# Performance work log

Hardware: AMD Instinct MI355X
Metric: run time of the kernel (lower is better)

The kernel has to match this reference:

```python
import jax, jax.numpy as jnp
import numpy as np

NUM_QUBITS = 13
NUM_LAYERS = 2


def setup_inputs() -> dict:
    key = jax.random.key(0)
    k1, k2 = jax.random.split(key)
    x = jax.random.normal(k1, (512, 2 ** NUM_QUBITS), dtype=jnp.float32)
    weights = jax.random.normal(k2, (NUM_LAYERS, NUM_QUBITS, 3), dtype=jnp.float32)
    return {"x": x, "weights": weights}


def _rot_matrix(phi, theta, omega):
    # qml.Rot(phi, theta, omega) = RZ(omega) @ RY(theta) @ RZ(phi)
    c = jnp.cos(theta * 0.5).astype(jnp.complex64)
    s = jnp.sin(theta * 0.5).astype(jnp.complex64)
    e_m = jnp.exp((-0.5j) * (phi + omega).astype(jnp.complex64))
    e_p = jnp.exp((0.5j) * (phi + omega).astype(jnp.complex64))
    e_d = jnp.exp((0.5j) * (phi - omega).astype(jnp.complex64))
    e_dc = jnp.exp((-0.5j) * (phi - omega).astype(jnp.complex64))
    row0 = jnp.stack([e_m * c, -e_d * s])
    row1 = jnp.stack([e_dc * s, e_p * c])
    return jnp.stack([row0, row1])  # (2, 2) complex64


def _apply_1q(psi, U, q):
    # psi: (B, 2, 2, ..., 2); contract qubit axis q with 2x2 gate U
    ax = 1 + q
    psi = jnp.moveaxis(psi, ax, -1)
    psi = psi @ U.T
    return jnp.moveaxis(psi, -1, ax)


def _apply_cnot(psi, c, t):
    # X on target where control bit == 1
    s0 = jax.lax.index_in_dim(psi, 0, axis=1 + c, keepdims=True)
    s1 = jax.lax.index_in_dim(psi, 1, axis=1 + c, keepdims=True)
    s1 = jnp.flip(s1, axis=1 + t)
    return jnp.concatenate([s0, s1], axis=1 + c)


def reference(x, weights):
    n = NUM_QUBITS
    B = x.shape[0]
    # AmplitudeEmbedding with normalize=True
    norm = jnp.sqrt(jnp.sum(x * x, axis=1, keepdims=True))
    psi = (x / norm).astype(jnp.complex64).reshape((B,) + (2,) * n)
    # StronglyEntanglingLayers (default ranges r_l = (l % (n-1)) + 1, CNOT imprimitive)
    for l in range(NUM_LAYERS):
        r = (l % (n - 1)) + 1
        for q in range(n):
            U = _rot_matrix(weights[l, q, 0], weights[l, q, 1], weights[l, q, 2])
            psi = _apply_1q(psi, U, q)
        for q in range(n):
            psi = _apply_cnot(psi, q, (q + r) % n)
    # expval(PauliZ(n // 2)) = p(bit=0) - p(bit=1)
    m = n // 2
    probs = jnp.real(psi) ** 2 + jnp.imag(psi) ** 2
    axes = tuple(i for i in range(1, n + 1) if i != 1 + m)
    p = probs.sum(axis=axes)  # (B, 2)
    return p[:, 0] - p[:, 1]
```

## Files before the change

kernel.cpp:

```cpp
#include <hip/hip_runtime.h>
#include <math.h>

#define NQ    13
#define DIM   8192
#define BLOCK 256
#define NGATE 26

#define SW_PAD(i) ((i) + (((i) >> 5) << 2))
#define LDS_N (DIM + 4 * (DIM / 32))

struct PCols { int c[NQ]; };
constexpr PCols make_cols(int r) {
    PCols P{};
    for (int b = 0; b < NQ; ++b) {
        int cc = 1 << b;
        for (int cq = 0; cq < NQ; ++cq) {
            const int cb = 12 - cq;
            const int tb = 12 - ((cq + r) % NQ);
            cc ^= ((cc >> cb) & 1) << tb;
        }
        P.c[b] = cc;
    }
    return P;
}
constexpr PCols C1 = make_cols(1);
constexpr PCols C2 = make_cols(2);
constexpr int make_rm6() {
    int m = 0;
    for (int b = 0; b < NQ; ++b) m |= ((make_cols(2).c[b] >> 6) & 1) << b;
    return m;
}
constexpr int RM6 = make_rm6();

template<int P>
__device__ __forceinline__ void rot32(float* vr, float* vi, const float* __restrict__ g) {
    const float u00r = g[0], u00i = g[1], u01r = g[2], u01i = g[3];
    const float u10r = g[4], u10i = g[5], u11r = g[6], u11i = g[7];
    #pragma unroll
    for (int m = 0; m < 16; ++m) {
        const int j0 = ((m >> P) << (P + 1)) | (m & ((1 << P) - 1));
        const int j1 = j0 | (1 << P);
        const float a0r = vr[j0], a0i = vi[j0];
        const float a1r = vr[j1], a1i = vi[j1];
        vr[j0] = u00r * a0r - u00i * a0i + u01r * a1r - u01i * a1i;
        vi[j0] = u00r * a0i + u00i * a0r + u01r * a1i + u01i * a1r;
        vr[j1] = u10r * a0r - u10i * a0i + u11r * a1r - u11i * a1i;
        vi[j1] = u10r * a0i + u10i * a0r + u11r * a1i + u11i * a1r;
    }
}

__device__ __forceinline__ void lds_load8x4(const float* arr, int base, int step, float* v) {
    #pragma unroll
    for (int g = 0; g < 8; ++g) {
        const float4 t = *(const float4*)&arr[base + step * g];
        v[4*g+0] = t.x; v[4*g+1] = t.y; v[4*g+2] = t.z; v[4*g+3] = t.w;
    }
}
__device__ __forceinline__ void lds_store8x4(float* arr, int base, int step, const float* v) {
    #pragma unroll
    for (int g = 0; g < 8; ++g) {
        float4 t;
        t.x = v[4*g+0]; t.y = v[4*g+1]; t.z = v[4*g+2]; t.w = v[4*g+3];
        *(float4*)&arr[base + step * g] = t;
    }
}

__global__ __launch_bounds__(BLOCK, 1) void qsim_kernel(
    const float* __restrict__ x,
    const float* __restrict__ w,
    float* __restrict__ out)
{
    __shared__ float re[LDS_N];
    __shared__ float im[LDS_N];
    __shared__ float gm[NGATE * 8];
    __shared__ float red[BLOCK / 64];

    const int b   = blockIdx.x;
    const int tid = threadIdx.x;

    if (tid < NGATE) {
        const float phi   = w[tid * 3 + 0];
        const float theta = w[tid * 3 + 1];
        const float omega = w[tid * 3 + 2];
        float c, s;  sincosf(0.5f * theta, &s, &c);
        float sps, cps, sds, cds;
        sincosf(0.5f * (phi + omega), &sps, &cps);
        sincosf(0.5f * (phi - omega), &sds, &cds);
        float* g = &gm[tid * 8];
        g[0] =  cps * c;  g[1] = -sps * c;
        g[2] = -cds * s;  g[3] = -sds * s;
        g[4] =  cds * s;  g[5] = -sds * s;
        g[6] =  cps * c;  g[7] =  sps * c;
    }

    const float4* x4 = (const float4*)(x + (size_t)b * DIM);
    float ss = 0.f;
    #pragma unroll
    for (int k = 0; k < 8; ++k) {
        const int m = tid + BLOCK * k;
        const int a = SW_PAD(m * 4);
        const float4 v = x4[m];
        *(float4*)&re[a] = v;
        *(float4*)&im[a] = make_float4(0.f, 0.f, 0.f, 0.f);
        ss += v.x * v.x + v.y * v.y + v.z * v.z + v.w * v.w;
    }
    #pragma unroll
    for (int off = 32; off > 0; off >>= 1) ss += __shfl_down(ss, off, 64);
    if ((tid & 63) == 0) red[tid >> 6] = ss;
    __syncthreads();
    const float total = red[0] + red[1] + red[2] + red[3];

    float vr[32], vi[32];
    const int baseA = 36 * tid;
    const int baseB = (tid >> 5) * 1152 + (tid & 31);
    const int baseC = 4 * tid + 4 * (tid >> 3);

    lds_load8x4(re, baseA, 4, vr);  lds_load8x4(im, baseA, 4, vi);
    rot32<0>(vr, vi, &gm[(0*13+12)*8]);
    rot32<1>(vr, vi, &gm[(0*13+11)*8]);
    rot32<2>(vr, vi, &gm[(0*13+10)*8]);
    rot32<3>(vr, vi, &gm[(0*13+ 9)*8]);
    rot32<4>(vr, vi, &gm[(0*13+ 8)*8]);
    lds_store8x4(re, baseA, 4, vr); lds_store8x4(im, baseA, 4, vi);
    __syncthreads();

    #pragma unroll
    for (int j = 0; j < 32; ++j) { vr[j] = re[baseB + 36*j]; vi[j] = im[baseB + 36*j]; }
    rot32<0>(vr, vi, &gm[(0*13+7)*8]);
    rot32<1>(vr, vi, &gm[(0*13+6)*8]);
    rot32<2>(vr, vi, &gm[(0*13+5)*8]);
    rot32<3>(vr, vi, &gm[(0*13+4)*8]);
    rot32<4>(vr, vi, &gm[(0*13+3)*8]);
    #pragma unroll
    for (int j = 0; j < 32; ++j) { re[baseB + 36*j] = vr[j]; im[baseB + 36*j] = vi[j]; }
    __syncthreads();

    lds_load8x4(re, baseC, 1152, vr);  lds_load8x4(im, baseC, 1152, vi);
    rot32<2>(vr, vi, &gm[(0*13+2)*8]);
    rot32<3>(vr, vi, &gm[(0*13+1)*8]);
    rot32<4>(vr, vi, &gm[(0*13+0)*8]);
    __syncthreads();
    {
        int tbase = 0;
        #pragma unroll
        for (int bb = 2; bb < 10; ++bb) if ((tid >> (bb - 2)) & 1) tbase ^= C1.c[bb];
        #pragma unroll
        for (int j = 0; j < 32; ++j) {
            int dest = tbase;
            if (j & 1)  dest ^= C1.c[0];
            if (j & 2)  dest ^= C1.c[1];
            if (j & 4)  dest ^= C1.c[10];
            if (j & 8)  dest ^= C1.c[11];
            if (j & 16) dest ^= C1.c[12];
            const int a = SW_PAD(dest);
            re[a] = vr[j]; im[a] = vi[j];
        }
    }
    __syncthreads();

    lds_load8x4(re, baseA, 4, vr);  lds_load8x4(im, baseA, 4, vi);
    rot32<0>(vr, vi, &gm[(1*13+12)*8]);
    rot32<1>(vr, vi, &gm[(1*13+11)*8]);
    rot32<2>(vr, vi, &gm[(1*13+10)*8]);
    rot32<3>(vr, vi, &gm[(1*13+ 9)*8]);
    rot32<4>(vr, vi, &gm[(1*13+ 8)*8]);
    lds_store8x4(re, baseA, 4, vr); lds_store8x4(im, baseA, 4, vi);
    __syncthreads();

    #pragma unroll
    for (int j = 0; j < 32; ++j) { vr[j] = re[baseB + 36*j]; vi[j] = im[baseB + 36*j]; }
    rot32<0>(vr, vi, &gm[(1*13+7)*8]);
    rot32<1>(vr, vi, &gm[(1*13+6)*8]);
    rot32<2>(vr, vi, &gm[(1*13+5)*8]);
    rot32<3>(vr, vi, &gm[(1*13+4)*8]);
    rot32<4>(vr, vi, &gm[(1*13+3)*8]);
    #pragma unroll
    for (int j = 0; j < 32; ++j) { re[baseB + 36*j] = vr[j]; im[baseB + 36*j] = vi[j]; }
    __syncthreads();

    lds_load8x4(re, baseC, 1152, vr);  lds_load8x4(im, baseC, 1152, vi);
    rot32<2>(vr, vi, &gm[(1*13+2)*8]);
    rot32<3>(vr, vi, &gm[(1*13+1)*8]);
    rot32<4>(vr, vi, &gm[(1*13+0)*8]);

    float acc = 0.f;
    #pragma unroll
    for (int jh = 0; jh < 8; ++jh) {
        #pragma unroll
        for (int jl = 0; jl < 4; ++jl) {
            const int j = jh * 4 + jl;
            const int i = (jh << 10) | (tid << 2) | jl;
            const float pr = vr[j] * vr[j] + vi[j] * vi[j];
            acc += (__popc(i & RM6) & 1) ? -pr : pr;
        }
    }
    #pragma unroll
    for (int off = 32; off > 0; off >>= 1) acc += __shfl_down(acc, off, 64);
    __syncthreads();
    if ((tid & 63) == 0) red[tid >> 6] = acc;
    __syncthreads();
    if (tid == 0) out[b] = (red[0] + red[1] + red[2] + red[3]) / total;
}

extern "C" void kernel_launch(void* const* d_in, const int* in_sizes, int n_in,
                              void* d_out, int out_size, void* d_ws, size_t ws_size,
                              hipStream_t stream) {
    const float* x = (const float*)d_in[0];
    const float* w = (const float*)d_in[1];
    float* out = (float*)d_out;
    const int B = in_sizes[0] / DIM;
    qsim_kernel<<<B, BLOCK, 0, stream>>>(x, w, out);
}
```

Baseline: 88.97 us.

## Rewrite statevector kernel with 512 threads, XOR swizzle, DPP lane gates, separate gate prep

Doubles the block to 512 threads with 16 amplitudes per thread and applies two qubits per pass through DPP lane exchanges instead of holding them in registers. The padded LDS layout becomes an XOR swizzle, and the pass structure is redone to fit the new mapping. Gate matrices are now built in a separate prep kernel into workspace and read from global memory, with launch bounds allowing 4 blocks per CU. This targets register pressure and occupancy at the cost of a second launch and more cross-lane shuffles.

```diff
diff --git a/kernel.cpp b/kernel.cpp
--- a/kernel.cpp
+++ b/kernel.cpp
@@ -3,11 +3,13 @@
 
 #define NQ    13
 #define DIM   8192
-#define BLOCK 256
+#define BLOCK 512
 #define NGATE 26
 
-#define SW_PAD(i) ((i) + (((i) >> 5) << 2))
-#define LDS_N (DIM + 4 * (DIM / 32))
+__device__ __forceinline__ int SWZ(int i) {
+    return i ^ (((((i >> 4) ^ (i >> 6)) & 3)) << 2)
+             ^ ((((i >> 10) ^ (i >> 11)) & 1) << 4);
+}
 
 struct PCols { int c[NQ]; };
 constexpr PCols make_cols(int r) {
@@ -24,7 +26,6 @@
     return P;
 }
 constexpr PCols C1 = make_cols(1);
-constexpr PCols C2 = make_cols(2);
 constexpr int make_rm6() {
     int m = 0;
     for (int b = 0; b < NQ; ++b) m |= ((make_cols(2).c[b] >> 6) & 1) << b;
@@ -32,73 +33,147 @@
 }
 constexpr int RM6 = make_rm6();
 
+struct Combos { int k[16]; };
+constexpr Combos make_combos() {
+    Combos K{};
+    for (int j = 0; j < 16; ++j)
+        K.k[j] = ((j & 1) ? C1.c[0] : 0) ^ ((j & 2) ? C1.c[1] : 0)
+               ^ ((j & 4) ? C1.c[2] : 0) ^ ((j & 8) ? C1.c[12] : 0);
+    return K;
+}
+constexpr Combos KC = make_combos();
+
+struct G8 { float4 a, b; };
+
 template<int P>
-__device__ __forceinline__ void rot32(float* vr, float* vi, const float* __restrict__ g) {
-    const float u00r = g[0], u00i = g[1], u01r = g[2], u01i = g[3];
-    const float u10r = g[4], u10i = g[5], u11r = g[6], u11i = g[7];
-    #pragma unroll
-    for (int m = 0; m < 16; ++m) {
+__device__ __forceinline__ void rot16(float* vr, float* vi, const G8 g) {
+    #pragma unroll
+    for (int m = 0; m < 8; ++m) {
         const int j0 = ((m >> P) << (P + 1)) | (m & ((1 << P) - 1));
         const int j1 = j0 | (1 << P);
         const float a0r = vr[j0], a0i = vi[j0];
         const float a1r = vr[j1], a1i = vi[j1];
-        vr[j0] = u00r * a0r - u00i * a0i + u01r * a1r - u01i * a1i;
-        vi[j0] = u00r * a0i + u00i * a0r + u01r * a1i + u01i * a1r;
-        vr[j1] = u10r * a0r - u10i * a0i + u11r * a1r - u11i * a1i;
-        vi[j1] = u10r * a0i + u10i * a0r + u11r * a1i + u11i * a1r;
-    }
-}
-
-__device__ __forceinline__ void lds_load8x4(const float* arr, int base, int step, float* v) {
-    #pragma unroll
-    for (int g = 0; g < 8; ++g) {
-        const float4 t = *(const float4*)&arr[base + step * g];
-        v[4*g+0] = t.x; v[4*g+1] = t.y; v[4*g+2] = t.z; v[4*g+3] = t.w;
-    }
-}
-__device__ __forceinline__ void lds_store8x4(float* arr, int base, int step, const float* v) {
-    #pragma unroll
-    for (int g = 0; g < 8; ++g) {
-        float4 t;
-        t.x = v[4*g+0]; t.y = v[4*g+1]; t.z = v[4*g+2]; t.w = v[4*g+3];
-        *(float4*)&arr[base + step * g] = t;
-    }
-}
-
-__global__ __launch_bounds__(BLOCK, 1) void qsim_kernel(
-    const float* __restrict__ x,
-    const float* __restrict__ w,
-    float* __restrict__ out)
-{
-    __shared__ float re[LDS_N];
-    __shared__ float im[LDS_N];
-    __shared__ float gm[NGATE * 8];
-    __shared__ float red[BLOCK / 64];
-
-    const int b   = blockIdx.x;
-    const int tid = threadIdx.x;
-
-    if (tid < NGATE) {
-        const float phi   = w[tid * 3 + 0];
-        const float theta = w[tid * 3 + 1];
-        const float omega = w[tid * 3 + 2];
+        vr[j0] = g.a.x * a0r - g.a.y * a0i + g.a.z * a1r - g.a.w * a1i;
+        vi[j0] = g.a.x * a0i + g.a.y * a0r + g.a.z * a1i + g.a.w * a1r;
+        vr[j1] = g.b.x * a0r - g.b.y * a0i + g.b.z * a1r - g.b.w * a1i;
+        vi[j1] = g.b.x * a0i + g.b.y * a0r + g.b.z * a1i + g.b.w * a1r;
+    }
+}
+
+template<int CTRL>
+__device__ __forceinline__ float dppx(float v) {
+    return __int_as_float(
+        __builtin_amdgcn_update_dpp(0, __float_as_int(v), CTRL, 0xf, 0xf, true));
+}
+
+template<int CTRL>
+__device__ __forceinline__ void rotlane16(float* vr, float* vi, const G8 g, const bool hi) {
+    const float Ar = hi ? g.b.z : g.a.x;
+    const float Ai = hi ? g.b.w : g.a.y;
+    const float Br = hi ? g.b.x : g.a.z;
+    const float Bi = hi ? g.b.y : g.a.w;
+    #pragma unroll
+    for (int j = 0; j < 16; ++j) {
+        const float pr = dppx<CTRL>(vr[j]);
+        const float pi = dppx<CTRL>(vi[j]);
+        const float orr = vr[j], oii = vi[j];
+        vr[j] = Ar * orr - Ai * oii + Br * pr - Bi * pi;
+        vi[j] = Ar * oii + Ai * orr + Br * pi + Bi * pr;
+    }
+}
+
+__device__ __forceinline__ void passA(float* re, float* im, const G8* __restrict__ gw,
+                                      const int l, const int t) {
+    float vr[16], vi[16];
+    const int base = t << 4;
+    #pragma unroll
+    for (int g = 0; g < 4; ++g) {
+        const int a = SWZ(base + 4 * g);
+        *(float4*)&vr[4 * g] = *(const float4*)&re[a];
+        *(float4*)&vi[4 * g] = *(const float4*)&im[a];
+    }
+    rot16<0>(vr, vi, gw[l * 13 + 12]);
+    rot16<1>(vr, vi, gw[l * 13 + 11]);
+    rot16<2>(vr, vi, gw[l * 13 + 10]);
+    rot16<3>(vr, vi, gw[l * 13 +  9]);
+    rotlane16<0xB1>(vr, vi, gw[l * 13 + 8], (t & 1) != 0);
+    rotlane16<0x4E>(vr, vi, gw[l * 13 + 7], (t & 2) != 0);
+    #pragma unroll
+    for (int g = 0; g < 4; ++g) {
+        const int a = SWZ(base + 4 * g);
+        *(float4*)&re[a] = *(const float4*)&vr[4 * g];
+        *(float4*)&im[a] = *(const float4*)&vi[4 * g];
+    }
+}
+
+__device__ __forceinline__ void passB(float* re, float* im, const G8* __restrict__ gw,
+                                      const int l, const int t) {
+    float vr[16], vi[16];
+    const int base = ((t >> 8) << 12) | ((t & 3) << 10) | ((t >> 2) & 63);
+    const int sb = SWZ(base);
+    #pragma unroll
+    for (int j = 0; j < 16; ++j) {
+        const int a = sb ^ (j << 6) ^ ((j & 3) << 2);
+        vr[j] = re[a]; vi[j] = im[a];
+    }
+    rot16<0>(vr, vi, gw[l * 13 + 6]);
+    rot16<1>(vr, vi, gw[l * 13 + 5]);
+    rot16<2>(vr, vi, gw[l * 13 + 4]);
+    rot16<3>(vr, vi, gw[l * 13 + 3]);
+    rotlane16<0xB1>(vr, vi, gw[l * 13 + 2], (t & 1) != 0);
+    rotlane16<0x4E>(vr, vi, gw[l * 13 + 1], (t & 2) != 0);
+    #pragma unroll
+    for (int j = 0; j < 16; ++j) {
+        const int a = sb ^ (j << 6) ^ ((j & 3) << 2);
+        re[a] = vr[j]; im[a] = vi[j];
+    }
+}
+
+__device__ __forceinline__ void passC_load(const float* re, const float* im,
+                                           float* vr, float* vi, const int t) {
+    #pragma unroll
+    for (int h = 0; h < 2; ++h)
+        #pragma unroll
+        for (int k = 0; k < 2; ++k) {
+            const int a = SWZ((h << 12) | (t << 3) | (k << 2));
+            *(float4*)&vr[h * 8 + 4 * k] = *(const float4*)&re[a];
+            *(float4*)&vi[h * 8 + 4 * k] = *(const float4*)&im[a];
+        }
+}
+
+__global__ void prep_gates(const float* __restrict__ w, G8* __restrict__ gw) {
+    const int t = threadIdx.x;
+    if (t < NGATE) {
+        const float phi = w[t * 3 + 0], theta = w[t * 3 + 1], omega = w[t * 3 + 2];
         float c, s;  sincosf(0.5f * theta, &s, &c);
         float sps, cps, sds, cds;
         sincosf(0.5f * (phi + omega), &sps, &cps);
         sincosf(0.5f * (phi - omega), &sds, &cds);
-        float* g = &gm[tid * 8];
-        g[0] =  cps * c;  g[1] = -sps * c;
-        g[2] = -cds * s;  g[3] = -sds * s;
-        g[4] =  cds * s;  g[5] = -sds * s;
-        g[6] =  cps * c;  g[7] =  sps * c;
-    }
+        G8 g;
+        g.a = make_float4(cps * c, -sps * c, -cds * s, -sds * s);
+        g.b = make_float4(cds * s, -sds * s,  cps * c,  sps * c);
+        gw[t] = g;
+    }
+}
+
+__global__ __launch_bounds__(BLOCK, 4) void qsim_kernel(
+    const float* __restrict__ x,
+    const G8* __restrict__ gw,
+    float* __restrict__ out)
+{
+    __shared__ float re[DIM];
+    __shared__ float im[DIM];
+    __shared__ float red[BLOCK / 64];
+
+    const int b = blockIdx.x;
+    const int t = threadIdx.x;
 
     const float4* x4 = (const float4*)(x + (size_t)b * DIM);
     float ss = 0.f;
     #pragma unroll
-    for (int k = 0; k < 8; ++k) {
-        const int m = tid + BLOCK * k;
-        const int a = SW_PAD(m * 4);
+    for (int k = 0; k < 4; ++k) {
+        const int m = t + BLOCK * k;
+        const int a = SWZ(4 * m);
         const float4 v = x4[m];
         *(float4*)&re[a] = v;
         *(float4*)&im[a] = make_float4(0.f, 0.f, 0.f, 0.f);
@@ -106,100 +181,59 @@
     }
     #pragma unroll
     for (int off = 32; off > 0; off >>= 1) ss += __shfl_down(ss, off, 64);
-    if ((tid & 63) == 0) red[tid >> 6] = ss;
-    __syncthreads();
-    const float total = red[0] + red[1] + red[2] + red[3];
-
-    float vr[32], vi[32];
-    const int baseA = 36 * tid;
-    const int baseB = (tid >> 5) * 1152 + (tid & 31);
-    const int baseC = 4 * tid + 4 * (tid >> 3);
-
-    lds_load8x4(re, baseA, 4, vr);  lds_load8x4(im, baseA, 4, vi);
-    rot32<0>(vr, vi, &gm[(0*13+12)*8]);
-    rot32<1>(vr, vi, &gm[(0*13+11)*8]);
-    rot32<2>(vr, vi, &gm[(0*13+10)*8]);
-    rot32<3>(vr, vi, &gm[(0*13+ 9)*8]);
-    rot32<4>(vr, vi, &gm[(0*13+ 8)*8]);
-    lds_store8x4(re, baseA, 4, vr); lds_store8x4(im, baseA, 4, vi);
-    __syncthreads();
-
-    #pragma unroll
-    for (int j = 0; j < 32; ++j) { vr[j] = re[baseB + 36*j]; vi[j] = im[baseB + 36*j]; }
-    rot32<0>(vr, vi, &gm[(0*13+7)*8]);
-    rot32<1>(vr, vi, &gm[(0*13+6)*8]);
-    rot32<2>(vr, vi, &gm[(0*13+5)*8]);
-    rot32<3>(vr, vi, &gm[(0*13+4)*8]);
-    rot32<4>(vr, vi, &gm[(0*13+3)*8]);
-    #pragma unroll
-    for (int j = 0; j < 32; ++j) { re[baseB + 36*j] = vr[j]; im[baseB + 36*j] = vi[j]; }
-    __syncthreads();
-
-    lds_load8x4(re, baseC, 1152, vr);  lds_load8x4(im, baseC, 1152, vi);
-    rot32<2>(vr, vi, &gm[(0*13+2)*8]);
-    rot32<3>(vr, vi, &gm[(0*13+1)*8]);
-    rot32<4>(vr, vi, &gm[(0*13+0)*8]);
+    if ((t & 63) == 0) red[t >> 6] = ss;
+    __syncthreads();
+    float total = 0.f;
+    #pragma unroll
+    for (int i = 0; i < BLOCK / 64; ++i) total += red[i];
+
+    float vr[16], vi[16];
+
+    passA(re, im, gw, 0, t);
+    __syncthreads();
+    passB(re, im, gw, 0, t);
+    __syncthreads();
+    passC_load(re, im, vr, vi, t);
+    rot16<3>(vr, vi, gw[0 * 13 + 0]);
     __syncthreads();
     {
-        int tbase = 0;
-        #pragma unroll
-        for (int bb = 2; bb < 10; ++bb) if ((tid >> (bb - 2)) & 1) tbase ^= C1.c[bb];
-        #pragma unroll
-        for (int j = 0; j < 32; ++j) {
-            int dest = tbase;
-            if (j & 1)  dest ^= C1.c[0];
-            if (j & 2)  dest ^= C1.c[1];
-            if (j & 4)  dest ^= C1.c[10];
-            if (j & 8)  dest ^= C1.c[11];
-            if (j & 16) dest ^= C1.c[12];
-            const int a = SW_PAD(dest);
+        int tpart = 0;
+        #pragma unroll
+        for (int bb = 0; bb < 9; ++bb)
+            if ((t >> bb) & 1) tpart ^= C1.c[3 + bb];
+        #pragma unroll
+        for (int j = 0; j < 16; ++j) {
+            const int a = SWZ(tpart ^ KC.k[j]);
             re[a] = vr[j]; im[a] = vi[j];
         }
     }
     __syncthreads();
 
-    lds_load8x4(re, baseA, 4, vr);  lds_load8x4(im, baseA, 4, vi);
-    rot32<0>(vr, vi, &gm[(1*13+12)*8]);
-    rot32<1>(vr, vi, &gm[(1*13+11)*8]);
-    rot32<2>(vr, vi, &gm[(1*13+10)*8]);
-    rot32<3>(vr, vi, &gm[(1*13+ 9)*8]);
-    rot32<4>(vr, vi, &gm[(1*13+ 8)*8]);
-    lds_store8x4(re, baseA, 4, vr); lds_store8x4(im, baseA, 4, vi);
-    __syncthreads();
-
-    #pragma unroll
-    for (int j = 0; j < 32; ++j) { vr[j] = re[baseB + 36*j]; vi[j] = im[baseB + 36*j]; }
-    rot32<0>(vr, vi, &gm[(1*13+7)*8]);
-    rot32<1>(vr, vi, &gm[(1*13+6)*8]);
-    rot32<2>(vr, vi, &gm[(1*13+5)*8]);
-    rot32<3>(vr, vi, &gm[(1*13+4)*8]);
-    rot32<4>(vr, vi, &gm[(1*13+3)*8]);
-    #pragma unroll
-    for (int j = 0; j < 32; ++j) { re[baseB + 36*j] = vr[j]; im[baseB + 36*j] = vi[j]; }
-    __syncthreads();
-
-    lds_load8x4(re, baseC, 1152, vr);  lds_load8x4(im, baseC, 1152, vi);
-    rot32<2>(vr, vi, &gm[(1*13+2)*8]);
-    rot32<3>(vr, vi, &gm[(1*13+1)*8]);
-    rot32<4>(vr, vi, &gm[(1*13+0)*8]);
+    passA(re, im, gw, 1, t);
+    __syncthreads();
+    passB(re, im, gw, 1, t);
+    __syncthreads();
+    passC_load(re, im, vr, vi, t);
+    rot16<3>(vr, vi, gw[1 * 13 + 0]);
 
     float acc = 0.f;
     #pragma unroll
-    for (int jh = 0; jh < 8; ++jh) {
-        #pragma unroll
-        for (int jl = 0; jl < 4; ++jl) {
-            const int j = jh * 4 + jl;
-            const int i = (jh << 10) | (tid << 2) | jl;
-            const float pr = vr[j] * vr[j] + vi[j] * vi[j];
-            acc += (__popc(i & RM6) & 1) ? -pr : pr;
-        }
+    for (int j = 0; j < 16; ++j) {
+        const int i = ((j >> 3) << 12) | (t << 3) | (j & 7);
+        const float p = vr[j] * vr[j] + vi[j] * vi[j];
+        acc += (__popc(i & RM6) & 1) ? -p : p;
     }
     #pragma unroll
     for (int off = 32; off > 0; off >>= 1) acc += __shfl_down(acc, off, 64);
     __syncthreads();
-    if ((tid & 63) == 0) red[tid >> 6] = acc;
-    __syncthreads();
-    if (tid == 0) out[b] = (red[0] + red[1] + red[2] + red[3]) / total;
+    if ((t & 63) == 0) red[t >> 6] = acc;
+    __syncthreads();
+    if (t == 0) {
+        float tot = 0.f;
+        #pragma unroll
+        for (int i = 0; i < BLOCK / 64; ++i) tot += red[i];
+        out[b] = tot / total;
+    }
 }
 
 extern "C" void kernel_launch(void* const* d_in, const int* in_sizes, int n_in,
@@ -208,6 +242,8 @@
     const float* x = (const float*)d_in[0];
     const float* w = (const float*)d_in[1];
     float* out = (float*)d_out;
+    G8* gw = (G8*)d_ws;
     const int B = in_sizes[0] / DIM;
-    qsim_kernel<<<B, BLOCK, 0, stream>>>(x, w, out);
-}
+    prep_gates<<<1, 64, 0, stream>>>(w, gw);
+    qsim_kernel<<<B, BLOCK, 0, stream>>>(x, (const G8*)gw, out);
+}
```

Result: slower. 90.96 us (+2.2%).
